# Optimization experiments

Hardware: AMD Instinct MI355X
Metric: run time of the kernel (lower is better)

Reference implementation:

```python
import jax, jax.numpy as jnp
import numpy as np

N_NODES = 50000
N_EDGES = 800000
NODE_DIM = 64
EDGE_DIM = 32
HIDDEN_DIM = 128
OUT_DIM = 64


def setup_inputs() -> dict:
    key = jax.random.key(0)
    k1, k2, k3, k4, k5, k6, k7 = jax.random.split(key, 7)
    in_dim = EDGE_DIM + 2 * NODE_DIM  # 160
    edge_index = jax.random.randint(k1, (2, N_EDGES), 0, N_NODES, dtype=jnp.int64)
    node_features = jax.random.normal(k2, (N_NODES, NODE_DIM), dtype=jnp.float32)
    edge_features = jax.random.normal(k3, (N_EDGES, EDGE_DIM), dtype=jnp.float32)
    # MLP params (kaiming-uniform-ish init scale, values only matter for correctness testing)
    w1 = jax.random.normal(k4, (in_dim, HIDDEN_DIM), dtype=jnp.float32) * (1.0 / np.sqrt(in_dim))
    b1 = jax.random.normal(k5, (HIDDEN_DIM,), dtype=jnp.float32) * 0.01
    w2 = jax.random.normal(k6, (HIDDEN_DIM, OUT_DIM), dtype=jnp.float32) * (1.0 / np.sqrt(HIDDEN_DIM))
    b2 = jax.random.normal(k7, (OUT_DIM,), dtype=jnp.float32) * 0.01
    return {
        "edge_index": edge_index,
        "node_features": node_features,
        "edge_features": edge_features,
        "w1": w1, "b1": b1, "w2": w2, "b2": b2,
    }


def reference(edge_index, node_features, edge_features, w1, b1, w2, b2):
    # Gather source / target node features along the edge list: [E, NODE_DIM]
    src = node_features[edge_index[0]]
    tgt = node_features[edge_index[1]]
    # Concat to [E, EDGE_DIM + 2*NODE_DIM]
    x = jnp.concatenate([edge_features, src, tgt], axis=1)
    # 2-layer MLP: Linear -> ReLU -> Linear
    h = jax.nn.relu(x @ w1 + b1)
    return h @ w2 + b2
```

## Files before the change

kernel.cpp:

```cpp
#include <hip/hip_runtime.h>

#define E_TOTAL 800000
#define NN      50000
#define ND      64
#define ED      32
#define HD      128
#define OD      64
#define IND     160
#define MT      128
#define NTHREADS 512

typedef __attribute__((ext_vector_type(8))) short          short8;
typedef __attribute__((ext_vector_type(4))) float          f32x4;
typedef __attribute__((ext_vector_type(8))) unsigned short u16x8;
typedef __attribute__((ext_vector_type(4))) unsigned short u16x4;

__device__ __forceinline__ unsigned short f2bf(float f) {
  union { float f; unsigned u; } v; v.f = f;
  unsigned r = v.u + 0x7fffu + ((v.u >> 16) & 1u);
  return (unsigned short)(r >> 16);
}

#define X_FRAGS   40
#define SMEM_U16  ((X_FRAGS + 40) * 512)
#define SMEM_BYTES (SMEM_U16 * 2)

__global__ void cvt_nodes(const float* __restrict__ in, unsigned short* __restrict__ out, int n4) {
  int i = blockIdx.x * blockDim.x + threadIdx.x;
  const int stride = gridDim.x * blockDim.x;
  for (; i < n4; i += stride) {
    float4 v = ((const float4*)in)[i];
    u16x4 o = { f2bf(v.x), f2bf(v.y), f2bf(v.z), f2bf(v.w) };
    ((u16x4*)out)[i] = o;
  }
}

__global__ void pack_w1(const float* __restrict__ w, unsigned short* __restrict__ out) {
  int i = blockIdx.x * blockDim.x + threadIdx.x;
  if (i >= HD * IND) return;
  int j = i & 7, l = (i >> 3) & 63, f = i >> 9;
  int ks = f >> 3, t = f & 7;
  int k = ks * 32 + (l >> 4) * 8 + j;
  int n = t * 16 + (l & 15);
  out[i] = f2bf(w[k * HD + n]);
}

__global__ void pack_w2(const float* __restrict__ w, unsigned short* __restrict__ out) {
  int i = blockIdx.x * blockDim.x + threadIdx.x;
  if (i >= OD * HD) return;
  int j = i & 7, l = (i >> 3) & 63, f = i >> 9;
  int ks = f >> 2, t = f & 3;
  int k = ks * 32 + (l >> 4) * 8 + j;
  int n = t * 16 + (l & 15);
  out[i] = f2bf(w[k * OD + n]);
}

__global__ __launch_bounds__(NTHREADS, 4)
void edge_mlp(const int* __restrict__ eidx,
              const float* __restrict__ ef,
              const unsigned short* __restrict__ nbf,
              const unsigned short* __restrict__ w1p,
              const unsigned short* __restrict__ w2p,
              const float* __restrict__ b1,
              const float* __restrict__ b2,
              float* __restrict__ out)
{
  extern __shared__ unsigned short sm[];
  unsigned short* Xs = sm;
  unsigned short* W1 = sm + X_FRAGS * 512;

  const int  tid  = threadIdx.x;
  const long e0   = (long)blockIdx.x * MT;
  const int  wid  = tid >> 6;
  const int  lane = tid & 63;
  const int  lq   = lane >> 4;
  const int  lr   = lane & 15;

  const int  erow = wid * 16 + lr;
  const float4 efv0 = *(const float4*)(ef + (e0 + erow) * ED + lq * 8);
  const float4 efv1 = *(const float4*)(ef + (e0 + erow) * ED + lq * 8 + 4);

  u16x8 sv[2], tv[2];
  int   saddr[2], taddr[2];
  #pragma unroll
  for (int ii = 0; ii < 2; ++ii) {
    const int i = tid + ii * NTHREADS;
    const int f = i >> 6;
    const int w = f >> 1, kss = f & 1;
    const int l = i & 63;
    const int row = w * 16 + (l & 15);
    int s = eidx[e0 + row];
    s = s < 0 ? 0 : (s >= NN ? NN - 1 : s);
    sv[ii]   = *(const u16x8*)(nbf + (long)s * ND + kss * 32 + (l >> 4) * 8);
    saddr[ii] = ((w * 5 + 1 + kss) * 64 + l) * 8;
  }
  #pragma unroll
  for (int ii = 0; ii < 2; ++ii) {
    const int i = tid + ii * NTHREADS;
    const int f = i >> 6;
    const int w = f >> 1, kss = f & 1;
    const int l = i & 63;
    const int row = w * 16 + (l & 15);
    int t = eidx[E_TOTAL + e0 + row];
    t = t < 0 ? 0 : (t >= NN ? NN - 1 : t);
    tv[ii]   = *(const u16x8*)(nbf + (long)t * ND + kss * 32 + (l >> 4) * 8);
    taddr[ii] = ((w * 5 + 3 + kss) * 64 + l) * 8;
  }
  u16x8 wv[5];
  #pragma unroll
  for (int c = 0; c < 5; ++c)
    wv[c] = *(const u16x8*)(w1p + (tid + c * NTHREADS) * 8);

  float b1v[8];
  #pragma unroll
  for (int t = 0; t < 8; ++t) b1v[t] = b1[t * 16 + lr];
  float b2v[4];
  #pragma unroll
  for (int t = 0; t < 4; ++t) b2v[t] = b2[t * 16 + lr];

  {
    u16x8 o = { f2bf(efv0.x), f2bf(efv0.y), f2bf(efv0.z), f2bf(efv0.w),
                f2bf(efv1.x), f2bf(efv1.y), f2bf(efv1.z), f2bf(efv1.w) };
    *(u16x8*)(Xs + (wid * 5 + 0) * 512 + lane * 8) = o;
  }
  #pragma unroll
  for (int ii = 0; ii < 2; ++ii) *(u16x8*)(Xs + saddr[ii]) = sv[ii];
  #pragma unroll
  for (int ii = 0; ii < 2; ++ii) *(u16x8*)(Xs + taddr[ii]) = tv[ii];
  #pragma unroll
  for (int c = 0; c < 5; ++c)
    *(u16x8*)(W1 + (tid + c * NTHREADS) * 8) = wv[c];

  __syncthreads();

  f32x4 acc[8];
  #pragma unroll
  for (int t = 0; t < 8; ++t) acc[t] = (f32x4)0.0f;

  #pragma unroll
  for (int ks = 0; ks < 5; ++ks) {
    const short8 a = *(const short8*)(Xs + (wid * 5 + ks) * 512 + lane * 8);
    #pragma unroll
    for (int t = 0; t < 8; ++t) {
      const short8 b = *(const short8*)(W1 + (ks * 8 + t) * 512 + lane * 8);
      acc[t] = __builtin_amdgcn_mfma_f32_16x16x32_bf16(a, b, acc[t], 0, 0, 0);
    }
  }
  __syncthreads();

  #pragma unroll
  for (int t = 0; t < 8; ++t) {
    #pragma unroll
    for (int r = 0; r < 4; ++r) {
      float h = acc[t][r] + b1v[t];
      h = h > 0.0f ? h : 0.0f;
      const int k    = t * 16 + lr;
      const int frag = wid * 4 + (k >> 5);
      const int l2   = (((k >> 3) & 3) << 4) + lq * 4 + r;
      Xs[frag * 512 + l2 * 8 + (k & 7)] = f2bf(h);
    }
  }
  __syncthreads();

  short8 a2[4];
  #pragma unroll
  for (int ks = 0; ks < 4; ++ks)
    a2[ks] = *(const short8*)(Xs + (wid * 4 + ks) * 512 + lane * 8);

  f32x4 acc2[4];
  #pragma unroll
  for (int t = 0; t < 4; ++t) acc2[t] = (f32x4)0.0f;

  #pragma unroll
  for (int t = 0; t < 4; ++t) {
    #pragma unroll
    for (int ks = 0; ks < 4; ++ks) {
      const short8 b = *(const short8*)(w2p + ((ks * 4 + t) * 64 + lane) * 8);
      acc2[t] = __builtin_amdgcn_mfma_f32_16x16x32_bf16(a2[ks], b, acc2[t], 0, 0, 0);
    }
  }

  #pragma unroll
  for (int t = 0; t < 4; ++t) {
    #pragma unroll
    for (int r = 0; r < 4; ++r) {
      const long m = e0 + wid * 16 + lq * 4 + r;
      out[m * OD + t * 16 + lr] = acc2[t][r] + b2v[t];
    }
  }
}

extern "C" void kernel_launch(void* const* d_in, const int* in_sizes, int n_in,
                              void* d_out, int out_size, void* d_ws, size_t ws_size,
                              hipStream_t stream) {
  const int*   eidx = (const int*)d_in[0];
  const float* nf   = (const float*)d_in[1];
  const float* ef   = (const float*)d_in[2];
  const float* w1   = (const float*)d_in[3];
  const float* b1   = (const float*)d_in[4];
  const float* w2   = (const float*)d_in[5];
  const float* b2   = (const float*)d_in[6];
  float*       out  = (float*)d_out;

  unsigned short* nbf = (unsigned short*)d_ws;
  unsigned short* w1p = nbf + (long)NN * ND;
  unsigned short* w2p = w1p + (long)HD * IND;

  cvt_nodes<<<1024, 256, 0, stream>>>(nf, nbf, (NN * ND) / 4);
  pack_w1<<<(HD * IND + 255) / 256, 256, 0, stream>>>(w1, w1p);
  pack_w2<<<(OD * HD + 255) / 256, 256, 0, stream>>>(w2, w2p);

  hipFuncSetAttribute((const void*)edge_mlp,
                      hipFuncAttributeMaxDynamicSharedMemorySize, SMEM_BYTES);
  edge_mlp<<<E_TOTAL / MT, NTHREADS, SMEM_BYTES, stream>>>(
      eidx, ef, nbf, w1p, w2p, b1, b2, out);
}
```

Measured before the change: 125.6 us.

## Make edge MLP persistent with register-held gathers and next-tile prefetch

```diff
diff --git a/kernel.cpp b/kernel.cpp
--- a/kernel.cpp
+++ b/kernel.cpp
@@ -9,6 +9,8 @@
 #define IND     160
 #define MT      128
 #define NTHREADS 512
+#define NT      (E_TOTAL / MT)
+#define GRID    512
 
 typedef __attribute__((ext_vector_type(8))) short          short8;
 typedef __attribute__((ext_vector_type(4))) float          f32x4;
@@ -21,8 +23,8 @@
   return (unsigned short)(r >> 16);
 }
 
-#define X_FRAGS   40
-#define SMEM_U16  ((X_FRAGS + 40) * 512)
+#define H_FRAGS  32
+#define SMEM_U16 ((H_FRAGS + 40) * 512)
 #define SMEM_BYTES (SMEM_U16 * 2)
 
 __global__ void cvt_nodes(const float* __restrict__ in, unsigned short* __restrict__ out, int n4) {
@@ -66,50 +68,21 @@
               float* __restrict__ out)
 {
   extern __shared__ unsigned short sm[];
-  unsigned short* Xs = sm;
-  unsigned short* W1 = sm + X_FRAGS * 512;
-
-  const int  tid  = threadIdx.x;
-  const long e0   = (long)blockIdx.x * MT;
-  const int  wid  = tid >> 6;
-  const int  lane = tid & 63;
-  const int  lq   = lane >> 4;
-  const int  lr   = lane & 15;
-
-  const int  erow = wid * 16 + lr;
-  const float4 efv0 = *(const float4*)(ef + (e0 + erow) * ED + lq * 8);
-  const float4 efv1 = *(const float4*)(ef + (e0 + erow) * ED + lq * 8 + 4);
-
-  u16x8 sv[2], tv[2];
-  int   saddr[2], taddr[2];
+  unsigned short* Hs = sm;
+  unsigned short* W1 = sm + H_FRAGS * 512;
+
+  const int tid  = threadIdx.x;
+  const int wid  = tid >> 6;
+  const int lane = tid & 63;
+  const int lq   = lane >> 4;
+  const int lr   = lane & 15;
+  const int rowoff = wid * 16 + lr;
+
   #pragma unroll
-  for (int ii = 0; ii < 2; ++ii) {
-    const int i = tid + ii * NTHREADS;
-    const int f = i >> 6;
-    const int w = f >> 1, kss = f & 1;
-    const int l = i & 63;
-    const int row = w * 16 + (l & 15);
-    int s = eidx[e0 + row];
-    s = s < 0 ? 0 : (s >= NN ? NN - 1 : s);
-    sv[ii]   = *(const u16x8*)(nbf + (long)s * ND + kss * 32 + (l >> 4) * 8);
-    saddr[ii] = ((w * 5 + 1 + kss) * 64 + l) * 8;
-  }
-  #pragma unroll
-  for (int ii = 0; ii < 2; ++ii) {
-    const int i = tid + ii * NTHREADS;
-    const int f = i >> 6;
-    const int w = f >> 1, kss = f & 1;
-    const int l = i & 63;
-    const int row = w * 16 + (l & 15);
-    int t = eidx[E_TOTAL + e0 + row];
-    t = t < 0 ? 0 : (t >= NN ? NN - 1 : t);
-    tv[ii]   = *(const u16x8*)(nbf + (long)t * ND + kss * 32 + (l >> 4) * 8);
-    taddr[ii] = ((w * 5 + 3 + kss) * 64 + l) * 8;
-  }
-  u16x8 wv[5];
-  #pragma unroll
-  for (int c = 0; c < 5; ++c)
-    wv[c] = *(const u16x8*)(w1p + (tid + c * NTHREADS) * 8);
+  for (int c = 0; c < 5; ++c) {
+    const int i = tid + c * NTHREADS;
+    *(u16x8*)(W1 + i * 8) = *(const u16x8*)(w1p + i * 8);
+  }
 
   float b1v[8];
   #pragma unroll
@@ -118,74 +91,112 @@
   #pragma unroll
   for (int t = 0; t < 4; ++t) b2v[t] = b2[t * 16 + lr];
 
+  int tile = blockIdx.x;
+  short8 g0, g1, g2, g3;
+  float4 e0v, e1v;
   {
-    u16x8 o = { f2bf(efv0.x), f2bf(efv0.y), f2bf(efv0.z), f2bf(efv0.w),
-                f2bf(efv1.x), f2bf(efv1.y), f2bf(efv1.z), f2bf(efv1.w) };
-    *(u16x8*)(Xs + (wid * 5 + 0) * 512 + lane * 8) = o;
-  }
-  #pragma unroll
-  for (int ii = 0; ii < 2; ++ii) *(u16x8*)(Xs + saddr[ii]) = sv[ii];
-  #pragma unroll
-  for (int ii = 0; ii < 2; ++ii) *(u16x8*)(Xs + taddr[ii]) = tv[ii];
-  #pragma unroll
-  for (int c = 0; c < 5; ++c)
-    *(u16x8*)(W1 + (tid + c * NTHREADS) * 8) = wv[c];
-
-  __syncthreads();
-
-  f32x4 acc[8];
-  #pragma unroll
-  for (int t = 0; t < 8; ++t) acc[t] = (f32x4)0.0f;
-
-  #pragma unroll
-  for (int ks = 0; ks < 5; ++ks) {
-    const short8 a = *(const short8*)(Xs + (wid * 5 + ks) * 512 + lane * 8);
+    const long e = (long)tile * MT + rowoff;
+    int si = eidx[e];           si = si < 0 ? 0 : (si >= NN ? NN - 1 : si);
+    int ti = eidx[E_TOTAL + e]; ti = ti < 0 ? 0 : (ti >= NN ? NN - 1 : ti);
+    const unsigned short* sr = nbf + (long)si * ND;
+    const unsigned short* tr = nbf + (long)ti * ND;
+    g0 = *(const short8*)(sr + lq * 8);
+    g1 = *(const short8*)(sr + 32 + lq * 8);
+    g2 = *(const short8*)(tr + lq * 8);
+    g3 = *(const short8*)(tr + 32 + lq * 8);
+    e0v = *(const float4*)(ef + e * ED + lq * 8);
+    e1v = *(const float4*)(ef + e * ED + lq * 8 + 4);
+  }
+
+  asm volatile("s_waitcnt lgkmcnt(0)" ::: "memory");
+  __builtin_amdgcn_s_barrier();
+  __builtin_amdgcn_sched_barrier(0);
+
+  for (; tile < NT; tile += GRID) {
+    const int  tnext = (tile + GRID < NT) ? (tile + GRID) : tile;
+    const long en    = (long)tnext * MT + rowoff;
+    int sn = eidx[en];
+    int tn = eidx[E_TOTAL + en];
+
+    short8 aef;
+    aef[0] = (short)f2bf(e0v.x); aef[1] = (short)f2bf(e0v.y);
+    aef[2] = (short)f2bf(e0v.z); aef[3] = (short)f2bf(e0v.w);
+    aef[4] = (short)f2bf(e1v.x); aef[5] = (short)f2bf(e1v.y);
+    aef[6] = (short)f2bf(e1v.z); aef[7] = (short)f2bf(e1v.w);
+
+    f32x4 acc[8];
+    #pragma unroll
+    for (int t = 0; t < 8; ++t) acc[t] = (f32x4)0.0f;
+
+    #pragma unroll
+    for (int ks = 0; ks < 5; ++ks) {
+      const short8 a = (ks == 0) ? aef : (ks == 1) ? g0 : (ks == 2) ? g1
+                        : (ks == 3) ? g2 : g3;
+      #pragma unroll
+      for (int t = 0; t < 8; ++t) {
+        const short8 b = *(const short8*)(W1 + (ks * 8 + t) * 512 + lane * 8);
+        acc[t] = __builtin_amdgcn_mfma_f32_16x16x32_bf16(a, b, acc[t], 0, 0, 0);
+      }
+    }
+
+    asm volatile("s_waitcnt lgkmcnt(0)" ::: "memory");
+    __builtin_amdgcn_s_barrier();
+    __builtin_amdgcn_sched_barrier(0);
+
     #pragma unroll
     for (int t = 0; t < 8; ++t) {
-      const short8 b = *(const short8*)(W1 + (ks * 8 + t) * 512 + lane * 8);
-      acc[t] = __builtin_amdgcn_mfma_f32_16x16x32_bf16(a, b, acc[t], 0, 0, 0);
-    }
-  }
-  __syncthreads();
-
-  #pragma unroll
-  for (int t = 0; t < 8; ++t) {
-    #pragma unroll
-    for (int r = 0; r < 4; ++r) {
-      float h = acc[t][r] + b1v[t];
-      h = h > 0.0f ? h : 0.0f;
-      const int k    = t * 16 + lr;
-      const int frag = wid * 4 + (k >> 5);
-      const int l2   = (((k >> 3) & 3) << 4) + lq * 4 + r;
-      Xs[frag * 512 + l2 * 8 + (k & 7)] = f2bf(h);
-    }
-  }
-  __syncthreads();
-
-  short8 a2[4];
-  #pragma unroll
-  for (int ks = 0; ks < 4; ++ks)
-    a2[ks] = *(const short8*)(Xs + (wid * 4 + ks) * 512 + lane * 8);
-
-  f32x4 acc2[4];
-  #pragma unroll
-  for (int t = 0; t < 4; ++t) acc2[t] = (f32x4)0.0f;
-
-  #pragma unroll
-  for (int t = 0; t < 4; ++t) {
-    #pragma unroll
-    for (int ks = 0; ks < 4; ++ks) {
-      const short8 b = *(const short8*)(w2p + ((ks * 4 + t) * 64 + lane) * 8);
-      acc2[t] = __builtin_amdgcn_mfma_f32_16x16x32_bf16(a2[ks], b, acc2[t], 0, 0, 0);
-    }
-  }
-
-  #pragma unroll
-  for (int t = 0; t < 4; ++t) {
-    #pragma unroll
-    for (int r = 0; r < 4; ++r) {
-      const long m = e0 + wid * 16 + lq * 4 + r;
-      out[m * OD + t * 16 + lr] = acc2[t][r] + b2v[t];
+      #pragma unroll
+      for (int r = 0; r < 4; ++r) {
+        float h = acc[t][r] + b1v[t];
+        h = h > 0.0f ? h : 0.0f;
+        const int k    = t * 16 + lr;
+        const int frag = wid * 4 + (k >> 5);
+        const int l2   = (((k >> 3) & 3) << 4) + lq * 4 + r;
+        Hs[frag * 512 + l2 * 8 + (k & 7)] = f2bf(h);
+      }
+    }
+
+    asm volatile("s_waitcnt lgkmcnt(0)" ::: "memory");
+    __builtin_amdgcn_s_barrier();
+    __builtin_amdgcn_sched_barrier(0);
+
+    short8 a2[4];
+    #pragma unroll
+    for (int ks = 0; ks < 4; ++ks)
+      a2[ks] = *(const short8*)(Hs + (wid * 4 + ks) * 512 + lane * 8);
+
+    sn = sn < 0 ? 0 : (sn >= NN ? NN - 1 : sn);
+    tn = tn < 0 ? 0 : (tn >= NN ? NN - 1 : tn);
+    {
+      const unsigned short* sr = nbf + (long)sn * ND;
+      const unsigned short* tr = nbf + (long)tn * ND;
+      g0 = *(const short8*)(sr + lq * 8);
+      g1 = *(const short8*)(sr + 32 + lq * 8);
+      g2 = *(const short8*)(tr + lq * 8);
+      g3 = *(const short8*)(tr + 32 + lq * 8);
+      e0v = *(const float4*)(ef + en * ED + lq * 8);
+      e1v = *(const float4*)(ef + en * ED + lq * 8 + 4);
+    }
+
+    f32x4 acc2[4];
+    #pragma unroll
+    for (int t = 0; t < 4; ++t) acc2[t] = (f32x4)0.0f;
+    #pragma unroll
+    for (int t = 0; t < 4; ++t) {
+      #pragma unroll
+      for (int ks = 0; ks < 4; ++ks) {
+        const short8 b = *(const short8*)(w2p + ((ks * 4 + t) * 64 + lane) * 8);
+        acc2[t] = __builtin_amdgcn_mfma_f32_16x16x32_bf16(a2[ks], b, acc2[t], 0, 0, 0);
+      }
+    }
+
+    const long mbase = (long)tile * MT + wid * 16 + lq * 4;
+    #pragma unroll
+    for (int t = 0; t < 4; ++t) {
+      #pragma unroll
+      for (int r = 0; r < 4; ++r) {
+        out[(mbase + r) * OD + t * 16 + lr] = acc2[t][r] + b2v[t];
+      }
     }
   }
 }
@@ -212,6 +223,6 @@
 
   hipFuncSetAttribute((const void*)edge_mlp,
                       hipFuncAttributeMaxDynamicSharedMemorySize, SMEM_BYTES);
-  edge_mlp<<<E_TOTAL / MT, NTHREADS, SMEM_BYTES, stream>>>(
+  edge_mlp<<<GRID, NTHREADS, SMEM_BYTES, stream>>>(
       eidx, ef, nbf, w1p, w2p, b1, b2, out);
 }
```

New measurement: 140.4 us. +11.8%, slower.
